# Kernel tuning notes

Hardware: AMD Instinct MI355X
Metric: run time of the kernel (lower is better)

The kernel has to match this reference:

```python
import jax, jax.numpy as jnp
import numpy as np

D, E, DFF, TOPK = 768, 4, 1024, 2


def setup_inputs() -> dict:
    key = jax.random.key(0)
    ks = jax.random.split(key, 6)
    s = 0.02  # init scale for weights
    return {
        "input_ids": jax.random.normal(ks[0], (8, 2048, D), dtype=jnp.float32),
        "W": jax.random.normal(ks[1], (D, D), dtype=jnp.float32) * s,
        "b": jnp.zeros((D,), dtype=jnp.float32),
        "Wg": jax.random.normal(ks[2], (D, E), dtype=jnp.float32) * s,
        "bg": jnp.zeros((E,), dtype=jnp.float32),
        "W1": jax.random.normal(ks[3], (E, D, DFF), dtype=jnp.float32) * s,
        "b1": jnp.zeros((E, DFF), dtype=jnp.float32),
        "W2": jax.random.normal(ks[4], (E, DFF, D), dtype=jnp.float32) * s,
        "b2": jnp.zeros((E, D), dtype=jnp.float32),
    }


def reference(input_ids, W, b, Wg, bg, W1, b1, W2, b2):
    B, S, _ = input_ids.shape
    # Dense projection feeding the MoE layer
    h = jnp.einsum("bsd,de->bse", input_ids, W) + b          # [B,S,D]
    t = h.reshape(-1, D)                                      # [T,D] tokens

    # Token-choice router: softmax over experts, top-2, renormalized gates
    logits = t @ Wg + bg                                      # [T,E]
    probs = jax.nn.softmax(logits, axis=-1)
    vals, idx = jax.lax.top_k(probs, TOPK)                    # [T,K]
    gates = vals / jnp.sum(vals, axis=-1, keepdims=True)
    # Dense combine weights [T,E]: zero for non-selected experts
    comb = jnp.sum(jax.nn.one_hot(idx, E, dtype=t.dtype) * gates[..., None], axis=1)

    # Expert FFNs (E small -> compute all experts, weighted combine)
    pre = jnp.einsum("td,edf->etf", t, W1) + b1[:, None, :]   # [E,T,DFF]
    y_e = jnp.einsum("etf,efd->etd", jax.nn.gelu(pre), W2) + b2[:, None, :]
    out = jnp.einsum("te,etd->td", comb, y_e)                 # [T,D]
    return out.reshape(B, S, D)
```

## Files before the change

### kernel.cpp

```cpp
#include <hip/hip_runtime.h>

#define DIM 768
#define NEXP 4
#define DFF_ 1024
#define CAP 16384

typedef __attribute__((ext_vector_type(4))) float f32x4;
typedef __attribute__((ext_vector_type(8))) short s16x8;

__device__ __forceinline__ unsigned short f32_to_bf16(float f) {
  unsigned int u = __float_as_uint(f);
  unsigned int r = (u + 0x7FFFu + ((u >> 16) & 1u)) >> 16;
  return (unsigned short)r;
}
__device__ __forceinline__ float bf16_to_f32(unsigned short u) {
  return __uint_as_float(((unsigned int)u) << 16);
}
__device__ __forceinline__ unsigned lds_off(const void* p) {
  return (unsigned)(unsigned long long)(__attribute__((address_space(3))) const void*)p;
}

__global__ void pack_bf16_kernel(const float* __restrict__ in,
                                 unsigned short* __restrict__ out,
                                 int K, int C) {
  const int t = threadIdx.x;
  const int lane = t & 63;
  const int pb = blockIdx.x * 4 + (t >> 6);
  const int KT = K >> 5;
  const int n16 = pb / KT, kt = pb - n16 * KT;
  const int z = blockIdx.z;
  in  += (size_t)z * K * C;
  out += (size_t)z * K * C;
  const int col = n16 * 16 + (lane & 15);
  const int k0 = kt * 32 + (lane >> 4) * 8;
  s16x8 vv;
#pragma unroll
  for (int e = 0; e < 8; e++) vv[e] = (short)f32_to_bf16(in[(size_t)(k0 + e) * C + col]);
  *(s16x8*)(out + (size_t)pb * 512 + lane * 8) = vv;
}

__global__ void wfg_kernel(const float* __restrict__ W, const float* __restrict__ Wg,
                           const float* __restrict__ b, const float* __restrict__ bg,
                           float* __restrict__ wfg, float* __restrict__ bgp) {
  int gid = blockIdx.x * 256 + threadIdx.x;
  if (gid < DIM * NEXP) {
    int k = gid >> 2, e = gid & 3;
    const float* wr = W + (size_t)k * DIM;
    float acc = 0.f;
    for (int d = 0; d < DIM; d++) acc += wr[d] * Wg[d * NEXP + e];
    wfg[gid] = acc;
  } else if (gid < DIM * NEXP + NEXP) {
    int e = gid - DIM * NEXP;
    float acc = bg[e];
    for (int d = 0; d < DIM; d++) acc += b[d] * Wg[d * NEXP + e];
    bgp[e] = acc;
  }
}

__global__ void router_kernel(const float* __restrict__ x, const float* __restrict__ wfg,
                              const float* __restrict__ bgp,
                              int2* __restrict__ rte, float2* __restrict__ rtg,
                              unsigned short* __restrict__ xbf) {
  __shared__ float wfgS[DIM * NEXP];
  const int tid = threadIdx.x;
  for (int i = tid; i < DIM * NEXP; i += 256) wfgS[i] = wfg[i];
  __syncthreads();
  const int w = tid >> 6, lane = tid & 63;
  const size_t t = (size_t)blockIdx.x * 4 + w;
  const float* xr = x + t * DIM;
  unsigned short* xbr = xbf + t * DIM;
  float a0 = 0.f, a1 = 0.f, a2 = 0.f, a3 = 0.f;
#pragma unroll
  for (int i = 0; i < 6; i++) {
    int k = i * 128 + lane * 2;
    float2 xv = *(const float2*)(xr + k);
    ushort2 pk;
    pk.x = f32_to_bf16(xv.x);
    pk.y = f32_to_bf16(xv.y);
    *(ushort2*)(xbr + k) = pk;
    a0 += xv.x * wfgS[k * 4 + 0] + xv.y * wfgS[k * 4 + 4];
    a1 += xv.x * wfgS[k * 4 + 1] + xv.y * wfgS[k * 4 + 5];
    a2 += xv.x * wfgS[k * 4 + 2] + xv.y * wfgS[k * 4 + 6];
    a3 += xv.x * wfgS[k * 4 + 3] + xv.y * wfgS[k * 4 + 7];
  }
#pragma unroll
  for (int off = 32; off > 0; off >>= 1) {
    a0 += __shfl_xor(a0, off);
    a1 += __shfl_xor(a1, off);
    a2 += __shfl_xor(a2, off);
    a3 += __shfl_xor(a3, off);
  }
  if (lane == 0) {
    float l[NEXP] = {a0 + bgp[0], a1 + bgp[1], a2 + bgp[2], a3 + bgp[3]};
    float m = fmaxf(fmaxf(l[0], l[1]), fmaxf(l[2], l[3]));
    float p[NEXP]; float s = 0.f;
#pragma unroll
    for (int e = 0; e < NEXP; e++) { p[e] = expf(l[e] - m); s += p[e]; }
#pragma unroll
    for (int e = 0; e < NEXP; e++) p[e] /= s;
    int i1 = 0;
#pragma unroll
    for (int e = 1; e < NEXP; e++) if (p[e] > p[i1]) i1 = e;
    int i2 = -1;
#pragma unroll
    for (int e = 0; e < NEXP; e++) { if (e == i1) continue; if (i2 < 0 || p[e] > p[i2]) i2 = e; }
    float denom = p[i1] + p[i2];
    rte[t] = make_int2(i1, i2);
    rtg[t] = make_float2(p[i1] / denom, p[i2] / denom);
  }
}

__global__ void assign_kernel(const int2* __restrict__ rte, const float2* __restrict__ rtg,
                              int* __restrict__ cnt, int* __restrict__ idx_tok,
                              float* __restrict__ gate_sel, int2* __restrict__ tok_slot) {
  __shared__ int hist[NEXP];
  __shared__ int base[NEXP];
  const int tid = threadIdx.x;
  if (tid < NEXP) hist[tid] = 0;
  __syncthreads();
  const int t = blockIdx.x * 256 + tid;
  int2 e = rte[t];
  float2 g = rtg[t];
  int r1 = atomicAdd(&hist[e.x], 1);
  int r2 = atomicAdd(&hist[e.y], 1);
  __syncthreads();
  if (tid < NEXP) base[tid] = atomicAdd(&cnt[tid], hist[tid]);
  __syncthreads();
  int s1 = base[e.x] + r1, s2 = base[e.y] + r2;
  idx_tok[e.x * CAP + s1] = t;  gate_sel[e.x * CAP + s1] = g.x;
  idx_tok[e.y * CAP + s2] = t;  gate_sel[e.y * CAP + s2] = g.y;
  tok_slot[t] = make_int2((e.x << 14) | s1, (e.y << 14) | s2);
}

__global__ void combine_kernel(const unsigned short* __restrict__ y,
                               const int2* __restrict__ tok_slot,
                               const float2* __restrict__ rtg,
                               const int* __restrict__ cnts,
                               const float* __restrict__ b2,
                               float* __restrict__ out) {
  __shared__ float b2S[NEXP * DIM];
  const int tid = threadIdx.x;
  for (int i = tid; i < NEXP * DIM; i += 256) b2S[i] = b2[i];
  const int t0 = (cnts[0] + 127) >> 7, t1 = (cnts[1] + 127) >> 7, t2 = (cnts[2] + 127) >> 7;
  const int rb[NEXP] = {0, t0 * 128, (t0 + t1) * 128, (t0 + t1 + t2) * 128};
  __syncthreads();
  const int w = tid >> 6, lane = tid & 63;
  const size_t t = (size_t)blockIdx.x * 4 + w;
  int2 v = tok_slot[t];
  float2 cg = rtg[t];
  const int e1 = v.x >> 14, s1 = v.x & (CAP - 1);
  const int e2 = v.y >> 14, s2 = v.y & (CAP - 1);
  const unsigned short* y1 = y + (size_t)(rb[e1] + s1) * DIM;
  const unsigned short* y2 = y + (size_t)(rb[e2] + s2) * DIM;
  float* op = out + t * DIM;
  const float* bp1 = b2S + e1 * DIM;
  const float* bp2 = b2S + e2 * DIM;
#pragma unroll
  for (int k = 0; k < 12; k++) {
    int n = k * 64 + lane;
    op[n] = bf16_to_f32(y1[n]) + bf16_to_f32(y2[n]) + cg.x * bp1[n] + cg.y * bp2[n];
  }
}

template <int MODE, int CH, int NT>
__launch_bounds__(256, 3)
__global__ void gemm_kernel(const unsigned short* __restrict__ A, const int lda,
                            const unsigned short* __restrict__ Bp, const int ldb,
                            const int N,
                            const float* __restrict__ bias,
                            const int* __restrict__ idx_tok,
                            const float* __restrict__ gate_sel,
                            const int* __restrict__ cnts,
                            unsigned short* __restrict__ outB, const int ldo) {
  const int lin = blockIdx.y * gridDim.x + blockIdx.x;
  const int nT = gridDim.x;
  const int xcd = lin & 7, t8 = lin >> 3;
  int bn = 0, bm0 = 0;
  int bmLoc = 0, cnt = 1 << 30, segBase = 0, gRow0 = 0;
  const unsigned short* Bt = Bp;

  if constexpr (MODE == 0) {
    const int perXcd = gridDim.y >> 3;
    const int mi = t8 % CH;
    const int rest = t8 / CH;
    bn = rest % nT;
    const int mc = rest / nT;
    bm0 = (xcd * perXcd + mc * CH + mi) * 128;
  } else {
    const int c0 = cnts[0], c1 = cnts[1], c2 = cnts[2], c3 = cnts[3];
    const int t0 = (c0 + 127) >> 7, t1 = (c1 + 127) >> 7,
              t2 = (c2 + 127) >> 7, t3 = (c3 + 127) >> 7;
    const int p1 = t0, p2 = p1 + t1, p3 = p2 + t2, tot = p3 + t3;
    const int perXcd = (tot + 7) >> 3;
    bn = t8 % nT;
    const int mloc = t8 / nT;
    if (mloc >= perXcd) return;
    const int mIdx = xcd * perXcd + mloc;
    if (mIdx >= tot) return;
    const int seg = (mIdx >= p2) ? ((mIdx >= p3) ? 3 : 2) : ((mIdx >= p1) ? 1 : 0);
    const int pre = (seg == 3) ? p3 : (seg == 2) ? p2 : (seg == 1) ? p1 : 0;
    bmLoc = (mIdx - pre) * 128;
    segBase = seg * CAP;
    gRow0 = mIdx * 128;
    cnt = (seg == 3) ? c3 : (seg == 2) ? c2 : (seg == 1) ? c1 : c0;
    Bt += (size_t)seg * N * ldb;
    if constexpr (MODE == 1) bias += (size_t)seg * N;
  }

  __shared__ unsigned short As[3][128 * 32];
  __shared__ int idxS[128];
  __shared__ float gateS[128];

  const int tid = threadIdx.x;
  const int w = tid >> 6;
  const int lane = tid & 63;

  if constexpr (MODE == 1) {
    if (tid < 128) {
      int r = bmLoc + tid;
      int cl = (r < cnt) ? r : bmLoc;
      idxS[tid] = idx_tok[segBase + cl];
      gateS[tid] = gate_sel[segBase + cl];
    }
    __syncthreads();
  }

  const int r0 = tid >> 2, r1 = 64 + r0;
  const int gq = (tid & 3) ^ (r0 & 3);
  const unsigned short *aP0, *aP1;
  if constexpr (MODE == 0) {
    aP0 = A + (size_t)(bm0 + r0) * lda + gq * 8;
    aP1 = A + (size_t)(bm0 + r1) * lda + gq * 8;
  } else if constexpr (MODE == 1) {
    aP0 = A + (size_t)idxS[r0] * lda + gq * 8;
    aP1 = A + (size_t)idxS[r1] * lda + gq * 8;
  } else {
    aP0 = A + (size_t)(gRow0 + r0) * lda + gq * 8;
    aP1 = A + (size_t)(gRow0 + r1) * lda + gq * 8;
  }

  const int quad = lane >> 4;
  const int m16 = lane & 15;
  const int wm = (w & 1) * 64;
  const int wn = (w >> 1) * 64;
  const int sw = (quad ^ (m16 & 3)) * 16;

  const unsigned aBase0 = lds_off(&As[0][0]);
  const unsigned aRd = (unsigned)((wm + m16) * 64 + sw);

  const unsigned short* bp0 = Bt + (size_t)(bn * 8 + (w >> 1) * 4 + 0) * NT * 512 + lane * 8;
  const unsigned short* bp1 = Bt + (size_t)(bn * 8 + (w >> 1) * 4 + 1) * NT * 512 + lane * 8;
  const unsigned short* bp2 = Bt + (size_t)(bn * 8 + (w >> 1) * 4 + 2) * NT * 512 + lane * 8;
  const unsigned short* bp3 = Bt + (size_t)(bn * 8 + (w >> 1) * 4 + 3) * NT * 512 + lane * 8;

  f32x4 acc[4][4];
#pragma unroll
  for (int i = 0; i < 4; i++)
#pragma unroll
    for (int j = 0; j < 4; j++) acc[i][j] = (f32x4){0.f, 0.f, 0.f, 0.f};

  s16x8 br0[4], br1[4];

#define GLL(src, dst)                                                              \
  __builtin_amdgcn_global_load_lds((const __attribute__((address_space(1))) void*)(src), \
                                   (__attribute__((address_space(3))) void*)(dst), 16, 0, 0)
#define ISSUE_A(off, kk)                                                 \
  {                                                                      \
    char* la0 = (char*)&As[0][0] + (off) + w * 1024;                     \
    GLL(aP0 + (kk), la0);                                                \
    GLL(aP1 + (kk), la0 + 4096);                                         \
  }
#define LOADB(SET)                                                                   \
  {                                                                                  \
    asm volatile("global_load_dwordx4 %0, %1, off" : "=v"(br##SET[0]) : "v"(bp0));   \
    asm volatile("global_load_dwordx4 %0, %1, off" : "=v"(br##SET[1]) : "v"(bp1));   \
    asm volatile("global_load_dwordx4 %0, %1, off" : "=v"(br##SET[2]) : "v"(bp2));   \
    asm volatile("global_load_dwordx4 %0, %1, off" : "=v"(br##SET[3]) : "v"(bp3));   \
    bp0 += 512; bp1 += 512; bp2 += 512; bp3 += 512;                                  \
  }
#define DSR(dst, addr, imm) \
  asm volatile("ds_read_b128 %0, %1 offset:" #imm : "=v"(dst) : "v"(addr))
#define KSTEP(GATE, SET)                                                     \
  {                                                                          \
    asm volatile("s_waitcnt vmcnt(" #GATE ")" ::: "memory");                 \
    __builtin_amdgcn_sched_barrier(0);                                       \
    __builtin_amdgcn_s_barrier();                                            \
    asm volatile("" ::: "memory");                                           \
    s16x8 af[4];                                                             \
    const unsigned aAd = aBase0 + curOff + aRd;                              \
    DSR(af[0], aAd, 0);                                                      \
    DSR(af[1], aAd, 1024);                                                   \
    DSR(af[2], aAd, 2048);                                                   \
    DSR(af[3], aAd, 3072);                                                   \
    asm volatile("s_waitcnt lgkmcnt(0)" ::: "memory");                       \
    __builtin_amdgcn_sched_barrier(0);                                       \
    __builtin_amdgcn_s_barrier();                                            \
    asm volatile("" ::: "memory");                                           \
    __builtin_amdgcn_s_setprio(1);                                           \
    _Pragma("unroll") for (int i_ = 0; i_ < 4; i_++)                         \
    _Pragma("unroll") for (int j_ = 0; j_ < 4; j_++)                         \
      acc[i_][j_] = __builtin_amdgcn_mfma_f32_16x16x32_bf16(af[i_], br##SET[j_], \
                                                            acc[i_][j_], 0, 0, 0); \
    __builtin_amdgcn_s_setprio(0);                                           \
    curOff = (curOff == 16384u) ? 0u : curOff + 8192u;                       \
  }

  ISSUE_A(0, 0);
  LOADB(0);
  ISSUE_A(8192, 32);
  unsigned curOff = 0;
  unsigned stOff = 16384;
  int kk = 64;

  static_assert(NT >= 4 && (NT & 1) == 0, "NT must be even, >= 4");
#pragma unroll 1
  for (int ii = 0; ii < (NT - 2) / 2; ii++) {
    LOADB(1);
    ISSUE_A(stOff, kk);
    kk += 32;
    stOff = (stOff == 16384u) ? 0u : stOff + 8192u;
    KSTEP(8, 0);
    LOADB(0);
    ISSUE_A(stOff, kk);
    kk += 32;
    stOff = (stOff == 16384u) ? 0u : stOff + 8192u;
    KSTEP(8, 1);
  }
  LOADB(1);
  KSTEP(6, 0);
  KSTEP(0, 1);

#undef KSTEP
#undef DSR
#undef LOADB
#undef ISSUE_A
#undef GLL

#pragma unroll
  for (int i = 0; i < 4; i++) {
    const int rloc = wm + i * 16 + quad * 4;
#pragma unroll
    for (int j = 0; j < 4; j++) {
      const int col = bn * 128 + wn + j * 16 + m16;
      if constexpr (MODE == 0) {
        float bv = bias[col];
#pragma unroll
        for (int r = 0; r < 4; r++)
          outB[(size_t)(bm0 + rloc + r) * ldo + col] = f32_to_bf16(acc[i][j][r] + bv);
      } else if constexpr (MODE == 1) {
        float bv = bias[col];
#pragma unroll
        for (int r = 0; r < 4; r++) {
          if (bmLoc + rloc + r < cnt) {
            float v = acc[i][j][r] + bv;
            float t3 = v + 0.044715f * v * v * v;
            float e2 = exp2f(t3 * 2.302208206984525f);
            float rc = __builtin_amdgcn_rcpf(1.0f + e2);
            float g = v - v * rc;
            outB[(size_t)(gRow0 + rloc + r) * ldo + col] = f32_to_bf16(g * gateS[rloc + r]);
          }
        }
      } else {
#pragma unroll
        for (int r = 0; r < 4; r++) {
          if (bmLoc + rloc + r < cnt)
            outB[(size_t)(gRow0 + rloc + r) * ldo + col] = f32_to_bf16(acc[i][j][r]);
        }
      }
    }
  }
}

extern "C" void kernel_launch(void* const* d_in, const int* in_sizes, int n_in,
                              void* d_out, int out_size, void* d_ws, size_t ws_size,
                              hipStream_t stream) {
  (void)in_sizes; (void)n_in; (void)out_size; (void)ws_size;
  const float* x  = (const float*)d_in[0];
  const float* W  = (const float*)d_in[1];
  const float* b  = (const float*)d_in[2];
  const float* Wg = (const float*)d_in[3];
  const float* bg = (const float*)d_in[4];
  const float* W1 = (const float*)d_in[5];
  const float* b1 = (const float*)d_in[6];
  const float* W2 = (const float*)d_in[7];
  const float* b2 = (const float*)d_in[8];
  float* out = (float*)d_out;
  char* ws = (char*)d_ws;

  unsigned short* tbf  = (unsigned short*)(ws + 0);
  unsigned short* w1p  = (unsigned short*)(ws + 25165824);
  unsigned short* w2p  = (unsigned short*)(ws + 31457280);
  float* wfg           = (float*)(ws + 37748736);
  float* bgp           = (float*)(ws + 37761024);
  int2*  rte           = (int2*)(ws + 37761280);
  float2* rtg          = (float2*)(ws + 37892352);
  int*   cnt           = (int*)(ws + 38023424);
  int*   idx_tok       = (int*)(ws + 38023680);
  float* gate_sel      = (float*)(ws + 38285824);
  int2*  tok_slot      = (int2*)(ws + 38547968);
  unsigned short* g    = (unsigned short*)(ws + 38679040);
  unsigned short* xbf  = (unsigned short*)(ws + 38679040);
  unsigned short* wp   = (unsigned short*)(ws + 63844864);
  unsigned short* y    = (unsigned short*)(ws + 106574336);

  hipMemsetAsync(cnt, 0, NEXP * sizeof(int), stream);
  pack_bf16_kernel<<<dim3(288, 1, 1), 256, 0, stream>>>(W, wp, 768, 768);
  pack_bf16_kernel<<<dim3(384, 1, 4), 256, 0, stream>>>(W1, w1p, 768, 1024);
  pack_bf16_kernel<<<dim3(384, 1, 4), 256, 0, stream>>>(W2, w2p, 1024, 768);
  wfg_kernel<<<13, 256, 0, stream>>>(W, Wg, b, bg, wfg, bgp);
  router_kernel<<<4096, 256, 0, stream>>>(x, wfg, bgp, rte, rtg, xbf);
  assign_kernel<<<64, 256, 0, stream>>>(rte, rtg, cnt, idx_tok, gate_sel, tok_slot);

  gemm_kernel<0, 8, 24><<<dim3(6, 128), 256, 0, stream>>>(
      xbf, 768, wp, 768, 768, b, nullptr, nullptr, nullptr, tbf, 768);
  gemm_kernel<1, 8, 24><<<dim3(8, 264), 256, 0, stream>>>(
      tbf, 768, w1p, 768, 1024, b1, idx_tok, gate_sel, cnt, g, 1024);
  gemm_kernel<2, 8, 32><<<dim3(6, 264), 256, 0, stream>>>(
      g, 1024, w2p, 1024, 768, nullptr, nullptr, nullptr, cnt, y, 768);
  combine_kernel<<<4096, 256, 0, stream>>>(y, tok_slot, rtg, cnt, b2, out);
}
```

Measured before the change: 376.7 us.

## Give each wave private A staging in LDS and drop block barriers in GEMM loop

Each wave now loads only the 64 A rows it consumes into its own triple-buffered LDS region, so the two s_barrier calls per k-step are removed and waves advance independently. The loop is fully unrolled with a three-deep register ring for B and vmcnt gating. The cost is that A rows are loaded twice, once by each of the two waves sharing a row block, and LDS use grows from 24KB to 48KB, which may lower occupancy and code size grows with NT.

```diff
diff --git a/kernel.cpp b/kernel.cpp
--- a/kernel.cpp
+++ b/kernel.cpp
@@ -207,7 +207,7 @@
     if constexpr (MODE == 1) bias += (size_t)seg * N;
   }
 
-  __shared__ unsigned short As[3][128 * 32];
+  __shared__ unsigned short As[4][3][2048];
   __shared__ int idxS[128];
   __shared__ float gateS[128];
 
@@ -225,33 +225,34 @@
     __syncthreads();
   }
 
-  const int r0 = tid >> 2, r1 = 64 + r0;
-  const int gq = (tid & 3) ^ (r0 & 3);
-  const unsigned short *aP0, *aP1;
-  if constexpr (MODE == 0) {
-    aP0 = A + (size_t)(bm0 + r0) * lda + gq * 8;
-    aP1 = A + (size_t)(bm0 + r1) * lda + gq * 8;
-  } else if constexpr (MODE == 1) {
-    aP0 = A + (size_t)idxS[r0] * lda + gq * 8;
-    aP1 = A + (size_t)idxS[r1] * lda + gq * 8;
-  } else {
-    aP0 = A + (size_t)(gRow0 + r0) * lda + gq * 8;
-    aP1 = A + (size_t)(gRow0 + r1) * lda + gq * 8;
-  }
-
   const int quad = lane >> 4;
   const int m16 = lane & 15;
   const int wm = (w & 1) * 64;
   const int wn = (w >> 1) * 64;
-  const int sw = (quad ^ (m16 & 3)) * 16;
-
-  const unsigned aBase0 = lds_off(&As[0][0]);
-  const unsigned aRd = (unsigned)((wm + m16) * 64 + sw);
-
-  const unsigned short* bp0 = Bt + (size_t)(bn * 8 + (w >> 1) * 4 + 0) * NT * 512 + lane * 8;
-  const unsigned short* bp1 = Bt + (size_t)(bn * 8 + (w >> 1) * 4 + 1) * NT * 512 + lane * 8;
-  const unsigned short* bp2 = Bt + (size_t)(bn * 8 + (w >> 1) * 4 + 2) * NT * 512 + lane * 8;
-  const unsigned short* bp3 = Bt + (size_t)(bn * 8 + (w >> 1) * 4 + 3) * NT * 512 + lane * 8;
+
+  const int lrow = lane >> 2;
+  const int lslot = (lane & 3) ^ (lrow & 3);
+  const unsigned short* aSrc[4];
+#pragma unroll
+  for (int q = 0; q < 4; q++) {
+    const int rw = q * 16 + lrow;
+    size_t grow;
+    if constexpr (MODE == 0) grow = (size_t)(bm0 + wm + rw);
+    else if constexpr (MODE == 1) grow = (size_t)idxS[wm + rw];
+    else grow = (size_t)(gRow0 + wm + rw);
+    aSrc[q] = A + grow * lda + lslot * 8;
+  }
+
+  const unsigned wBase = lds_off(&As[w][0][0]);
+  const unsigned aRd = (unsigned)(m16 * 64 + ((quad ^ (m16 & 3)) * 16));
+  const unsigned aAd0 = wBase + aRd;
+  const unsigned aAd1 = wBase + 4096u + aRd;
+  const unsigned aAd2 = wBase + 8192u + aRd;
+
+  const unsigned short* bq0 = Bt + (size_t)(bn * 8 + (w >> 1) * 4 + 0) * NT * 512 + lane * 8;
+  const unsigned short* bq1 = Bt + (size_t)(bn * 8 + (w >> 1) * 4 + 1) * NT * 512 + lane * 8;
+  const unsigned short* bq2 = Bt + (size_t)(bn * 8 + (w >> 1) * 4 + 2) * NT * 512 + lane * 8;
+  const unsigned short* bq3 = Bt + (size_t)(bn * 8 + (w >> 1) * 4 + 3) * NT * 512 + lane * 8;
 
   f32x4 acc[4][4];
 #pragma unroll
@@ -259,81 +260,63 @@
 #pragma unroll
     for (int j = 0; j < 4; j++) acc[i][j] = (f32x4){0.f, 0.f, 0.f, 0.f};
 
-  s16x8 br0[4], br1[4];
+  s16x8 br[3][4];
 
 #define GLL(src, dst)                                                              \
   __builtin_amdgcn_global_load_lds((const __attribute__((address_space(1))) void*)(src), \
                                    (__attribute__((address_space(3))) void*)(dst), 16, 0, 0)
-#define ISSUE_A(off, kk)                                                 \
+#define GLLA(kt_)                                                        \
   {                                                                      \
-    char* la0 = (char*)&As[0][0] + (off) + w * 1024;                     \
-    GLL(aP0 + (kk), la0);                                                \
-    GLL(aP1 + (kk), la0 + 4096);                                         \
-  }
-#define LOADB(SET)                                                                   \
-  {                                                                                  \
-    asm volatile("global_load_dwordx4 %0, %1, off" : "=v"(br##SET[0]) : "v"(bp0));   \
-    asm volatile("global_load_dwordx4 %0, %1, off" : "=v"(br##SET[1]) : "v"(bp1));   \
-    asm volatile("global_load_dwordx4 %0, %1, off" : "=v"(br##SET[2]) : "v"(bp2));   \
-    asm volatile("global_load_dwordx4 %0, %1, off" : "=v"(br##SET[3]) : "v"(bp3));   \
-    bp0 += 512; bp1 += 512; bp2 += 512; bp3 += 512;                                  \
+    char* d_ = (char*)&As[w][(kt_) % 3][0];                              \
+    GLL(aSrc[0] + (kt_) * 32, d_);                                       \
+    GLL(aSrc[1] + (kt_) * 32, d_ + 1024);                                \
+    GLL(aSrc[2] + (kt_) * 32, d_ + 2048);                                \
+    GLL(aSrc[3] + (kt_) * 32, d_ + 3072);                                \
+  }
+#define LOADB(kt_)                                                                             \
+  {                                                                                            \
+    asm volatile("global_load_dwordx4 %0, %1, off" : "=v"(br[(kt_) % 3][0]) : "v"(bq0 + (kt_) * 512)); \
+    asm volatile("global_load_dwordx4 %0, %1, off" : "=v"(br[(kt_) % 3][1]) : "v"(bq1 + (kt_) * 512)); \
+    asm volatile("global_load_dwordx4 %0, %1, off" : "=v"(br[(kt_) % 3][2]) : "v"(bq2 + (kt_) * 512)); \
+    asm volatile("global_load_dwordx4 %0, %1, off" : "=v"(br[(kt_) % 3][3]) : "v"(bq3 + (kt_) * 512)); \
   }
 #define DSR(dst, addr, imm) \
   asm volatile("ds_read_b128 %0, %1 offset:" #imm : "=v"(dst) : "v"(addr))
-#define KSTEP(GATE, SET)                                                     \
-  {                                                                          \
-    asm volatile("s_waitcnt vmcnt(" #GATE ")" ::: "memory");                 \
-    __builtin_amdgcn_sched_barrier(0);                                       \
-    __builtin_amdgcn_s_barrier();                                            \
-    asm volatile("" ::: "memory");                                           \
-    s16x8 af[4];                                                             \
-    const unsigned aAd = aBase0 + curOff + aRd;                              \
-    DSR(af[0], aAd, 0);                                                      \
-    DSR(af[1], aAd, 1024);                                                   \
-    DSR(af[2], aAd, 2048);                                                   \
-    DSR(af[3], aAd, 3072);                                                   \
-    asm volatile("s_waitcnt lgkmcnt(0)" ::: "memory");                       \
-    __builtin_amdgcn_sched_barrier(0);                                       \
-    __builtin_amdgcn_s_barrier();                                            \
-    asm volatile("" ::: "memory");                                           \
-    __builtin_amdgcn_s_setprio(1);                                           \
-    _Pragma("unroll") for (int i_ = 0; i_ < 4; i_++)                         \
-    _Pragma("unroll") for (int j_ = 0; j_ < 4; j_++)                         \
-      acc[i_][j_] = __builtin_amdgcn_mfma_f32_16x16x32_bf16(af[i_], br##SET[j_], \
-                                                            acc[i_][j_], 0, 0, 0); \
-    __builtin_amdgcn_s_setprio(0);                                           \
-    curOff = (curOff == 16384u) ? 0u : curOff + 8192u;                       \
-  }
-
-  ISSUE_A(0, 0);
-  LOADB(0);
-  ISSUE_A(8192, 32);
-  unsigned curOff = 0;
-  unsigned stOff = 16384;
-  int kk = 64;
-
-  static_assert(NT >= 4 && (NT & 1) == 0, "NT must be even, >= 4");
-#pragma unroll 1
-  for (int ii = 0; ii < (NT - 2) / 2; ii++) {
-    LOADB(1);
-    ISSUE_A(stOff, kk);
-    kk += 32;
-    stOff = (stOff == 16384u) ? 0u : stOff + 8192u;
-    KSTEP(8, 0);
-    LOADB(0);
-    ISSUE_A(stOff, kk);
-    kk += 32;
-    stOff = (stOff == 16384u) ? 0u : stOff + 8192u;
-    KSTEP(8, 1);
-  }
-  LOADB(1);
-  KSTEP(6, 0);
-  KSTEP(0, 1);
-
-#undef KSTEP
+#define KGATE(N) asm volatile("s_waitcnt vmcnt(" #N ")" ::: "memory")
+
+  GLLA(0); LOADB(0);
+  GLLA(1); LOADB(1);
+
+  static_assert(NT >= 4, "NT must be >= 4");
+#pragma unroll
+  for (int kt = 0; kt < NT; ++kt) {
+    if (kt + 2 < NT) { GLLA(kt + 2); LOADB(kt + 2); }
+    if (kt < NT - 2) { KGATE(16); }
+    else if (kt == NT - 2) { KGATE(8); }
+    else { KGATE(0); }
+    __builtin_amdgcn_sched_barrier(0);
+    s16x8 af[4];
+    const unsigned aAd = ((kt % 3) == 0) ? aAd0 : ((kt % 3) == 1) ? aAd1 : aAd2;
+    DSR(af[0], aAd, 0);
+    DSR(af[1], aAd, 1024);
+    DSR(af[2], aAd, 2048);
+    DSR(af[3], aAd, 3072);
+    asm volatile("s_waitcnt lgkmcnt(0)" ::: "memory");
+    __builtin_amdgcn_sched_barrier(0);
+    __builtin_amdgcn_s_setprio(1);
+#pragma unroll
+    for (int i_ = 0; i_ < 4; i_++)
+#pragma unroll
+      for (int j_ = 0; j_ < 4; j_++)
+        acc[i_][j_] = __builtin_amdgcn_mfma_f32_16x16x32_bf16(af[i_], br[kt % 3][j_],
+                                                              acc[i_][j_], 0, 0, 0);
+    __builtin_amdgcn_s_setprio(0);
+  }
+
+#undef KGATE
 #undef DSR
 #undef LOADB
-#undef ISSUE_A
+#undef GLLA
 #undef GLL
 
 #pragma unroll
```

Result: slower. 412.0 us (+9.4%).
